# Kernel optimization log

Hardware: AMD Instinct MI355X
Metric: run time of the kernel (lower is better)

## Reference

```python
import jax, jax.numpy as jnp
import numpy as np

QUERY_DIM = 512
CONTEXT_DIM = 768
HEADS = 8
DIM_HEAD = 64
INNER = HEADS * DIM_HEAD  # 512


def setup_inputs() -> dict:
    key = jax.random.key(0)
    ks = jax.random.split(key, 7)
    b, n, ctx = 8, 4096, 512
    s = 0.02
    return {
        "x": jax.random.normal(ks[0], (b, n, QUERY_DIM), jnp.float32),
        "context": jax.random.normal(ks[1], (b, ctx, CONTEXT_DIM), jnp.float32),
        "w_q": jax.random.normal(ks[2], (QUERY_DIM, INNER), jnp.float32) * s,
        "w_k": jax.random.normal(ks[3], (CONTEXT_DIM, INNER), jnp.float32) * s,
        "w_v": jax.random.normal(ks[4], (CONTEXT_DIM, INNER), jnp.float32) * s,
        "w_out": jax.random.normal(ks[5], (INNER, QUERY_DIM), jnp.float32) * s,
        "b_out": jax.random.normal(ks[6], (QUERY_DIM,), jnp.float32) * s,
    }


def reference(x, context, w_q, w_k, w_v, w_out, b_out):
    b, n, _ = x.shape
    ctx = context.shape[1]
    scale = DIM_HEAD ** -0.5
    # project and split heads: [b, h, len, d]
    q = (x @ w_q).reshape(b, n, HEADS, DIM_HEAD).transpose(0, 2, 1, 3)
    k = (context @ w_k).reshape(b, ctx, HEADS, DIM_HEAD).transpose(0, 2, 1, 3)
    v = (context @ w_v).reshape(b, ctx, HEADS, DIM_HEAD).transpose(0, 2, 1, 3)
    attn = jax.nn.softmax(jnp.einsum("bhnd,bhmd->bhnm", q, k) * scale, axis=-1)
    out = jnp.einsum("bhnm,bhmd->bhnd", attn, v)
    out = out.transpose(0, 2, 1, 3).reshape(b, n, INNER)
    return out @ w_out + b_out
```

## Files before the change

### kernel.cpp

```cpp
#include <hip/hip_runtime.h>
#include <hip/hip_bf16.h>
#include <stdint.h>

typedef __attribute__((ext_vector_type(4)))  float  f32x4;
typedef __attribute__((ext_vector_type(16))) float  f32x16;
typedef __attribute__((ext_vector_type(8)))  short  bf8;
typedef __attribute__((ext_vector_type(4)))  short  bf4;
typedef __attribute__((ext_vector_type(4)))  float  fvec4;
typedef __attribute__((ext_vector_type(4)))  unsigned uvec4;
typedef __attribute__((ext_vector_type(2)))  unsigned uvec2;

#define AS1 __attribute__((address_space(1)))
#define AS3 __attribute__((address_space(3)))

#if __has_builtin(__builtin_amdgcn_exp2f)
#define EXP2(x) __builtin_amdgcn_exp2f(x)
#else
#define EXP2(x) exp2f(x)
#endif

__device__ __forceinline__ short sbf(float f) {
  __hip_bfloat16 h = __float2bfloat16(f);
  return *reinterpret_cast<short*>(&h);
}

__device__ __forceinline__ unsigned pk2(float lo, float hi) {
  unsigned r;
  asm("v_cvt_pk_bf16_f32 %0, %1, %2" : "=v"(r) : "v"(lo), "v"(hi));
  return r;
}

__global__ __launch_bounds__(256) void cvt_both(const float* __restrict__ a,
                                                short* __restrict__ ao, int na,
                                                const float* __restrict__ b,
                                                short* __restrict__ bo, int nb) {
  int idx = blockIdx.x * 256 + threadIdx.x;
  int stride = gridDim.x * 256 * 8;
  for (int i = idx * 8; i < na; i += stride) {
    fvec4 v0 = *(const fvec4*)(a + i);
    fvec4 v1 = *(const fvec4*)(a + i + 4);
    uvec4 o;
    o[0] = pk2(v0[0], v0[1]);
    o[1] = pk2(v0[2], v0[3]);
    o[2] = pk2(v1[0], v1[1]);
    o[3] = pk2(v1[2], v1[3]);
    *(uvec4*)(ao + i) = o;
  }
  for (int i = idx * 8; i < nb; i += stride) {
    fvec4 v0 = *(const fvec4*)(b + i);
    fvec4 v1 = *(const fvec4*)(b + i + 4);
    uvec4 o;
    o[0] = pk2(v0[0], v0[1]);
    o[1] = pk2(v0[2], v0[3]);
    o[2] = pk2(v1[0], v1[1]);
    o[3] = pk2(v1[2], v1[3]);
    *(uvec4*)(bo + i) = o;
  }
}

__device__ __forceinline__ void tr_tile(const float* __restrict__ src,
                                        short* __restrict__ dst, int K,
                                        float scale, int kx, int ny) {
  __shared__ short t[64][65];
  const int k0 = kx * 64, n0 = ny * 64;
  const int tx = threadIdx.x & 15, ty = threadIdx.x >> 4;
  #pragma unroll
  for (int i = 0; i < 4; ++i) {
    int k = ty + i * 16;
    fvec4 v = *(const fvec4*)(src + (size_t)(k0 + k) * 512 + n0 + tx * 4);
    t[tx * 4 + 0][k] = sbf(v[0] * scale);
    t[tx * 4 + 1][k] = sbf(v[1] * scale);
    t[tx * 4 + 2][k] = sbf(v[2] * scale);
    t[tx * 4 + 3][k] = sbf(v[3] * scale);
  }
  __syncthreads();
  #pragma unroll
  for (int i = 0; i < 4; ++i) {
    int n = ty + i * 16;
    bf4 o = *(bf4*)&t[n][tx * 4];
    *(bf4*)(dst + (size_t)(n0 + n) * K + k0 + tx * 4) = o;
  }
}

__global__ __launch_bounds__(256)
void prep_weights(const float* __restrict__ wq, const float* __restrict__ wk,
                  const float* __restrict__ wv, const float* __restrict__ wo,
                  short* __restrict__ wqT, short* __restrict__ wkvT,
                  short* __restrict__ woT, float qscale) {
  int bx = blockIdx.x;
  if (bx < 64)        tr_tile(wq, wqT, 512, qscale, bx & 7, bx >> 3);
  else if (bx < 160)  { int l = bx - 64;  tr_tile(wk, wkvT,            768, 1.0f, l % 12, l / 12); }
  else if (bx < 256)  { int l = bx - 160; tr_tile(wv, wkvT + 512*768,  768, 1.0f, l % 12, l / 12); }
  else                { int l = bx - 256; tr_tile(wo, woT, 512, 1.0f, l & 7, l >> 3); }
}

template<int EPI>
__global__ __launch_bounds__(256, 3)
void gemm_nt(const short* __restrict__ A, const short* __restrict__ Bt,
             void* __restrict__ Cout, void* __restrict__ Cout2,
             const float* __restrict__ bias, int M, int N, int K) {
  __shared__ short As[2][4096];
  __shared__ short Bs[2][4096];
  const int tid = threadIdx.x;
  const int w = tid >> 6, l = tid & 63, g = l >> 4, c15 = l & 15;
  const int mbase = blockIdx.x * 128, nbase = blockIdx.y * 128;
  const int wr = (w >> 1) << 6, wc = (w & 1) << 6;

  f32x4 acc[4][4];
  #pragma unroll
  for (int mi = 0; mi < 4; ++mi)
    #pragma unroll
    for (int ni = 0; ni < 4; ++ni) acc[mi][ni] = (f32x4){0.f, 0.f, 0.f, 0.f};

  int rowS[2], loS[2];
  #pragma unroll
  for (int p = 0; p < 2; ++p) {
    int pb = p * 4096 + tid * 16;
    rowS[p] = pb >> 6;
    loS[p] = ((pb & 63) ^ ((rowS[p] & 3) << 4)) >> 1;
  }

  auto stage = [&](int ks, int b) {
    #pragma unroll
    for (int p = 0; p < 2; ++p) {
      const short* ga = A  + (size_t)(mbase + rowS[p]) * K + (ks << 5) + loS[p];
      const short* gb = Bt + (size_t)(nbase + rowS[p]) * K + (ks << 5) + loS[p];
      __builtin_amdgcn_global_load_lds((const AS1 void*)ga,
          (AS3 void*)(&As[b][p * 2048 + w * 512]), 16, 0, 0);
      __builtin_amdgcn_global_load_lds((const AS1 void*)gb,
          (AS3 void*)(&Bs[b][p * 2048 + w * 512]), 16, 0, 0);
    }
  };

  const int nk = K >> 5;
  stage(0, 0);
  int buf = 0;
  for (int ks = 0; ks < nk; ++ks) {
    asm volatile("s_waitcnt vmcnt(0)\ns_barrier" ::: "memory");
    if (ks + 1 < nk) stage(ks + 1, buf ^ 1);

    bf8 af[4], bfr[4];
    #pragma unroll
    for (int mi = 0; mi < 4; ++mi) {
      int row = wr + mi * 16 + c15;
      af[mi] = *(const bf8*)&As[buf][(row << 5) + ((g << 3) ^ ((row & 3) << 3))];
    }
    #pragma unroll
    for (int ni = 0; ni < 4; ++ni) {
      int row = wc + ni * 16 + c15;
      bfr[ni] = *(const bf8*)&Bs[buf][(row << 5) + ((g << 3) ^ ((row & 3) << 3))];
    }
    #pragma unroll
    for (int mi = 0; mi < 4; ++mi)
      #pragma unroll
      for (int ni = 0; ni < 4; ++ni)
        acc[mi][ni] = __builtin_amdgcn_mfma_f32_16x16x32_bf16(af[mi], bfr[ni], acc[mi][ni], 0, 0, 0);
    buf ^= 1;
  }

  if (EPI == 2) {
    short* Kb = (short*)Cout;
    short* Vt = (short*)Cout2;
    #pragma unroll
    for (int mi = 0; mi < 4; ++mi) {
      int row0 = mbase + wr + mi * 16 + (g << 2);
      int b = row0 >> 9, key0 = row0 & 511;
      #pragma unroll
      for (int ni = 0; ni < 4; ++ni) {
        int col = nbase + wc + ni * 16 + c15;
        if (col < 512) {
          int h = col >> 6, d = col & 63;
          size_t base = ((size_t)((b << 3) + h) << 15) + d;
          #pragma unroll
          for (int r = 0; r < 4; ++r)
            Kb[base + ((size_t)(key0 + r) << 6)] = sbf(acc[mi][ni][r]);
        } else {
          int cc = col - 512;
          int h = cc >> 6, d = cc & 63;
          size_t base = ((size_t)((b << 3) + h) << 15) + ((size_t)d << 9) + key0;
          bf4 o4;
          #pragma unroll
          for (int r = 0; r < 4; ++r) o4[r] = sbf(acc[mi][ni][r]);
          *(bf4*)&Vt[base] = o4;
        }
      }
    }
  } else {
    #pragma unroll
    for (int mi = 0; mi < 4; ++mi) {
      int row0 = mbase + wr + mi * 16 + (g << 2);
      #pragma unroll
      for (int ni = 0; ni < 4; ++ni) {
        int col = nbase + wc + ni * 16 + c15;
        #pragma unroll
        for (int r = 0; r < 4; ++r) {
          float v = acc[mi][ni][r];
          if (EPI == 1) {
            v += bias[col];
            ((float*)Cout)[(size_t)(row0 + r) * N + col] = v;
          } else {
            ((short*)Cout)[(size_t)(row0 + r) * N + col] = sbf(v);
          }
        }
      }
    }
  }
}

__global__ __launch_bounds__(512, 4)
void attn_fwd(const short* __restrict__ Q, const short* __restrict__ Kb,
              const short* __restrict__ Vt, short* __restrict__ O) {
  extern __shared__ short smem[];

  const int p = blockIdx.x;
  const int v = (p & 7) * 128 + (p >> 3);
  const int bh = v >> 4, qx = v & 15;
  const int tid = threadIdx.x;
  const int w = tid >> 6, l = tid & 63, q = l & 31, h2 = l >> 5;
  const int bb = bh >> 3, h = bh & 7;
  const size_t orow0 = (size_t)bb * 4096 + qx * 256;
  const size_t kvbase = (size_t)bh << 15;

  bf8 qf[4];
  #pragma unroll
  for (int ds = 0; ds < 4; ++ds)
    qf[ds] = *(const bf8*)(Q + (orow0 + w * 32 + q) * 512 + h * 64 + ds * 16 + 8 * h2);

  const int srow = tid >> 3;
  const int soff = (tid & 7) * 16;
  const int slo  = (soff ^ ((srow & 7) << 4)) >> 1;
  const short* srcK0 = Kb + kvbase + ((size_t)srow << 6) + slo;
  const short* srcV0 = Vt + kvbase + ((size_t)srow << 9) + slo;

#define STAGE(t) do { \
    __builtin_amdgcn_global_load_lds((const AS1 void*)(srcK0 + ((size_t)(t) << 12)), \
        (AS3 void*)(smem + ((t) & 1) * 4096 + tid * 8), 16, 0, 0); \
    __builtin_amdgcn_global_load_lds((const AS1 void*)(srcV0 + ((t) << 6)), \
        (AS3 void*)(smem + 8192 + ((t) & 1) * 4096 + tid * 8), 16, 0, 0); } while (0)

  f32x16 o[2];
  #pragma unroll
  for (int db = 0; db < 2; ++db)
    #pragma unroll
    for (int r = 0; r < 16; ++r) o[db][r] = 0.f;
  float ls0 = 0.f, ls1 = 0.f, ls2 = 0.f, ls3 = 0.f;

  STAGE(0);

  #pragma unroll 2
  for (int t = 0; t < 8; ++t) {
    asm volatile("s_waitcnt vmcnt(0)\ns_barrier" ::: "memory");
    if (t < 7) STAGE(t + 1);
    const short* Kt  = smem + (t & 1) * 4096;
    const short* Vtl = smem + 8192 + (t & 1) * 4096;

    f32x16 s[2];
    __builtin_amdgcn_s_setprio(1);
    #pragma unroll
    for (int kb = 0; kb < 2; ++kb) {
      #pragma unroll
      for (int r = 0; r < 16; ++r) s[kb][r] = 0.f;
      #pragma unroll
      for (int ds = 0; ds < 4; ++ds) {
        bf8 kf = *(const bf8*)&Kt[((kb * 32 + q) << 6) +
                                  ((ds * 16 + 8 * h2) ^ ((q & 7) << 3))];
        s[kb] = __builtin_amdgcn_mfma_f32_32x32x16_bf16(kf, qf[ds], s[kb], 0, 0, 0);
      }
    }
    __builtin_amdgcn_s_setprio(0);

    #pragma unroll
    for (int kb = 0; kb < 2; ++kb)
      #pragma unroll
      for (int r = 0; r < 16; r += 4) {
        float p0 = EXP2(s[kb][r]);
        float p1 = EXP2(s[kb][r + 1]);
        float p2 = EXP2(s[kb][r + 2]);
        float p3 = EXP2(s[kb][r + 3]);
        s[kb][r] = p0; s[kb][r + 1] = p1; s[kb][r + 2] = p2; s[kb][r + 3] = p3;
        ls0 += p0; ls1 += p1; ls2 += p2; ls3 += p3;
      }

    #pragma unroll
    for (int ks = 0; ks < 4; ++ks) {
      const int kb = ks >> 1, rb = (ks & 1) * 8;
      unsigned X = pk2(s[kb][rb + 0], s[kb][rb + 1]);
      unsigned Y = pk2(s[kb][rb + 2], s[kb][rb + 3]);
      unsigned Z = pk2(s[kb][rb + 4], s[kb][rb + 5]);
      unsigned W = pk2(s[kb][rb + 6], s[kb][rb + 7]);
      asm volatile("v_permlane32_swap_b32 %0, %1" : "+v"(X), "+v"(Z));
      asm volatile("v_permlane32_swap_b32 %0, %1" : "+v"(Y), "+v"(W));
      union { unsigned u[4]; bf8 b; } pf;
      pf.u[0] = X; pf.u[1] = Y; pf.u[2] = Z; pf.u[3] = W;
      __builtin_amdgcn_s_setprio(1);
      #pragma unroll
      for (int db = 0; db < 2; ++db) {
        bf8 vf = *(const bf8*)&Vtl[((db * 32 + q) << 6) +
                                   ((ks * 16 + 8 * h2) ^ ((q & 7) << 3))];
        o[db] = __builtin_amdgcn_mfma_f32_32x32x16_bf16(vf, pf.b, o[db], 0, 0, 0);
      }
      __builtin_amdgcn_s_setprio(0);
    }
  }
#undef STAGE

  float lsum = (ls0 + ls1) + (ls2 + ls3);
  float tot = lsum + __shfl_xor(lsum, 32);
  float rs = 1.0f / tot;
  short* Orow = O + (orow0 + w * 32 + q) * 512 + h * 64;
  #pragma unroll
  for (int db = 0; db < 2; ++db)
    #pragma unroll
    for (int rq = 0; rq < 4; ++rq) {
      int r = rq * 4;
      uvec2 u;
      u[0] = pk2(o[db][r] * rs,     o[db][r + 1] * rs);
      u[1] = pk2(o[db][r + 2] * rs, o[db][r + 3] * rs);
      *(uvec2*)&Orow[db * 32 + rq * 8 + h2 * 4] = u;
    }
}

extern "C" void kernel_launch(void* const* d_in, const int* in_sizes, int n_in,
                              void* d_out, int out_size, void* d_ws, size_t ws_size,
                              hipStream_t stream) {
  const float* x   = (const float*)d_in[0];
  const float* ctx = (const float*)d_in[1];
  const float* wq  = (const float*)d_in[2];
  const float* wk  = (const float*)d_in[3];
  const float* wv  = (const float*)d_in[4];
  const float* wo  = (const float*)d_in[5];
  const float* bo  = (const float*)d_in[6];
  float* out = (float*)d_out;

  char* ws = (char*)d_ws;
  short* xb   = (short*)(ws);
  short* ctxb = (short*)(ws + 33554432);
  short* wqT  = (short*)(ws + 39845888);
  short* wkvT = (short*)(ws + 40370176);
  short* woT  = (short*)(ws + 41943040);
  short* Qb   = (short*)(ws + 42467328);
  short* Kbf  = (short*)(ws + 76021760);
  short* Vtf  = (short*)(ws + 80216064);
  short* Ab   = (short*)(ws + 84410368);

  (void)hipFuncSetAttribute((const void*)attn_fwd,
                            hipFuncAttributeMaxDynamicSharedMemorySize, 32768);

  const float QSCALE = 0.18033688011f;

  cvt_both<<<2048, 256, 0, stream>>>(x, xb, 16777216, ctx, ctxb, 3145728);
  prep_weights<<<320, 256, 0, stream>>>(wq, wk, wv, wo, wqT, wkvT, woT, QSCALE);

  gemm_nt<0><<<dim3(256, 4), 256, 0, stream>>>(xb, wqT, Qb, nullptr, nullptr, 32768, 512, 512);
  gemm_nt<2><<<dim3(32, 8), 256, 0, stream>>>(ctxb, wkvT, Kbf, Vtf, nullptr, 4096, 1024, 768);
  attn_fwd<<<dim3(1024), 512, 32768, stream>>>(Qb, Kbf, Vtf, Ab);
  gemm_nt<1><<<dim3(256, 4), 256, 0, stream>>>(Ab, woT, out, nullptr, bo, 32768, 512, 512);
}
```

Before: 148.6 us.

## Fuse fp32-to-bf16 input conversion into GEMM A-tile staging

Removes the standalone conversion kernel for x and context. The projection GEMMs now read fp32 A tiles directly, convert them to bf16 in registers, and store them swizzled into LDS after the MFMA step. This avoids writing and re-reading bf16 copies of the activations. In exchange, A is fetched at twice the width per N-tile and staged through registers instead of asynchronous direct-to-LDS loads, which adds register pressure and weakens load/compute overlap.

```diff
diff --git a/kernel.cpp b/kernel.cpp
--- a/kernel.cpp
+++ b/kernel.cpp
@@ -28,34 +28,6 @@
   unsigned r;
   asm("v_cvt_pk_bf16_f32 %0, %1, %2" : "=v"(r) : "v"(lo), "v"(hi));
   return r;
-}
-
-__global__ __launch_bounds__(256) void cvt_both(const float* __restrict__ a,
-                                                short* __restrict__ ao, int na,
-                                                const float* __restrict__ b,
-                                                short* __restrict__ bo, int nb) {
-  int idx = blockIdx.x * 256 + threadIdx.x;
-  int stride = gridDim.x * 256 * 8;
-  for (int i = idx * 8; i < na; i += stride) {
-    fvec4 v0 = *(const fvec4*)(a + i);
-    fvec4 v1 = *(const fvec4*)(a + i + 4);
-    uvec4 o;
-    o[0] = pk2(v0[0], v0[1]);
-    o[1] = pk2(v0[2], v0[3]);
-    o[2] = pk2(v1[0], v1[1]);
-    o[3] = pk2(v1[2], v1[3]);
-    *(uvec4*)(ao + i) = o;
-  }
-  for (int i = idx * 8; i < nb; i += stride) {
-    fvec4 v0 = *(const fvec4*)(b + i);
-    fvec4 v1 = *(const fvec4*)(b + i + 4);
-    uvec4 o;
-    o[0] = pk2(v0[0], v0[1]);
-    o[1] = pk2(v0[2], v0[3]);
-    o[2] = pk2(v1[0], v1[1]);
-    o[3] = pk2(v1[2], v1[3]);
-    *(uvec4*)(bo + i) = o;
-  }
 }
 
 __device__ __forceinline__ void tr_tile(const float* __restrict__ src,
@@ -94,13 +66,15 @@
   else                { int l = bx - 256; tr_tile(wo, woT, 512, 1.0f, l & 7, l >> 3); }
 }
 
-template<int EPI>
+template<int EPI, bool AF32>
 __global__ __launch_bounds__(256, 3)
-void gemm_nt(const short* __restrict__ A, const short* __restrict__ Bt,
+void gemm_nt(const void* __restrict__ Av, const short* __restrict__ Bt,
              void* __restrict__ Cout, void* __restrict__ Cout2,
              const float* __restrict__ bias, int M, int N, int K) {
   __shared__ short As[2][4096];
   __shared__ short Bs[2][4096];
+  const short* A16 = (const short*)Av;
+  const float* A32 = (const float*)Av;
   const int tid = threadIdx.x;
   const int w = tid >> 6, l = tid & 63, g = l >> 4, c15 = l & 15;
   const int mbase = blockIdx.x * 128, nbase = blockIdx.y * 128;
@@ -120,24 +94,58 @@
     loS[p] = ((pb & 63) ^ ((rowS[p] & 3) << 4)) >> 1;
   }
 
-  auto stage = [&](int ks, int b) {
+  const int ar = tid >> 1, ac0 = (tid & 1) * 16, acl = (tid & 1) * 2;
+  short* wdst0 = &As[0][ar * 32 + 8 * ((acl + 0) ^ (ar & 3))];
+  short* wdst1 = &As[0][ar * 32 + 8 * ((acl + 1) ^ (ar & 3))];
+
+  auto stageB = [&](int ks, int b) {
     #pragma unroll
     for (int p = 0; p < 2; ++p) {
-      const short* ga = A  + (size_t)(mbase + rowS[p]) * K + (ks << 5) + loS[p];
       const short* gb = Bt + (size_t)(nbase + rowS[p]) * K + (ks << 5) + loS[p];
+      __builtin_amdgcn_global_load_lds((const AS1 void*)gb,
+          (AS3 void*)(&Bs[b][p * 2048 + w * 512]), 16, 0, 0);
+    }
+  };
+  auto stageA16 = [&](int ks, int b) {
+    #pragma unroll
+    for (int p = 0; p < 2; ++p) {
+      const short* ga = A16 + (size_t)(mbase + rowS[p]) * K + (ks << 5) + loS[p];
       __builtin_amdgcn_global_load_lds((const AS1 void*)ga,
           (AS3 void*)(&As[b][p * 2048 + w * 512]), 16, 0, 0);
-      __builtin_amdgcn_global_load_lds((const AS1 void*)gb,
-          (AS3 void*)(&Bs[b][p * 2048 + w * 512]), 16, 0, 0);
     }
   };
 
   const int nk = K >> 5;
-  stage(0, 0);
+  fvec4 a0, a1, a2, a3;
+  auto loadA32 = [&](int ks) {
+    const float* p = A32 + (size_t)(mbase + ar) * K + (ks << 5) + ac0;
+    a0 = *(const fvec4*)(p);
+    a1 = *(const fvec4*)(p + 4);
+    a2 = *(const fvec4*)(p + 8);
+    a3 = *(const fvec4*)(p + 12);
+  };
+  auto writeA32 = [&](int b) {
+    uvec4 w0, w1;
+    w0[0] = pk2(a0[0], a0[1]); w0[1] = pk2(a0[2], a0[3]);
+    w0[2] = pk2(a1[0], a1[1]); w0[3] = pk2(a1[2], a1[3]);
+    w1[0] = pk2(a2[0], a2[1]); w1[1] = pk2(a2[2], a2[3]);
+    w1[2] = pk2(a3[0], a3[1]); w1[3] = pk2(a3[2], a3[3]);
+    *(uvec4*)(wdst0 + b * 4096) = w0;
+    *(uvec4*)(wdst1 + b * 4096) = w1;
+  };
+
+  if (AF32) { loadA32(0); writeA32(0); }
+  else      { stageA16(0, 0); }
+  stageB(0, 0);
+
   int buf = 0;
   for (int ks = 0; ks < nk; ++ks) {
-    asm volatile("s_waitcnt vmcnt(0)\ns_barrier" ::: "memory");
-    if (ks + 1 < nk) stage(ks + 1, buf ^ 1);
+    asm volatile("s_waitcnt vmcnt(0) lgkmcnt(0)\ns_barrier" ::: "memory");
+    if (ks + 1 < nk) {
+      if (AF32) loadA32(ks + 1);
+      else      stageA16(ks + 1, buf ^ 1);
+      stageB(ks + 1, buf ^ 1);
+    }
 
     bf8 af[4], bfr[4];
     #pragma unroll
@@ -155,6 +163,8 @@
       #pragma unroll
       for (int ni = 0; ni < 4; ++ni)
         acc[mi][ni] = __builtin_amdgcn_mfma_f32_16x16x32_bf16(af[mi], bfr[ni], acc[mi][ni], 0, 0, 0);
+
+    if (AF32 && ks + 1 < nk) writeA32(buf ^ 1);
     buf ^= 1;
   }
 
@@ -333,8 +343,6 @@
   float* out = (float*)d_out;
 
   char* ws = (char*)d_ws;
-  short* xb   = (short*)(ws);
-  short* ctxb = (short*)(ws + 33554432);
   short* wqT  = (short*)(ws + 39845888);
   short* wkvT = (short*)(ws + 40370176);
   short* woT  = (short*)(ws + 41943040);
@@ -348,11 +356,10 @@
 
   const float QSCALE = 0.18033688011f;
 
-  cvt_both<<<2048, 256, 0, stream>>>(x, xb, 16777216, ctx, ctxb, 3145728);
   prep_weights<<<320, 256, 0, stream>>>(wq, wk, wv, wo, wqT, wkvT, woT, QSCALE);
 
-  gemm_nt<0><<<dim3(256, 4), 256, 0, stream>>>(xb, wqT, Qb, nullptr, nullptr, 32768, 512, 512);
-  gemm_nt<2><<<dim3(32, 8), 256, 0, stream>>>(ctxb, wkvT, Kbf, Vtf, nullptr, 4096, 1024, 768);
+  gemm_nt<0, true><<<dim3(256, 4), 256, 0, stream>>>(x, wqT, Qb, nullptr, nullptr, 32768, 512, 512);
+  gemm_nt<2, true><<<dim3(32, 8), 256, 0, stream>>>(ctx, wkvT, Kbf, Vtf, nullptr, 4096, 1024, 768);
   attn_fwd<<<dim3(1024), 512, 32768, stream>>>(Qb, Kbf, Vtf, Ab);
-  gemm_nt<1><<<dim3(256, 4), 256, 0, stream>>>(Ab, woT, out, nullptr, bo, 32768, 512, 512);
-}
+  gemm_nt<1, false><<<dim3(256, 4), 256, 0, stream>>>(Ab, woT, out, nullptr, bo, 32768, 512, 512);
+}
```

New measurement: 144.6 us. 1.03x faster.
